# Optimization experiments

Hardware: AMD Instinct MI355X
Metric: run time of the kernel (lower is better)

## Reference

```python
import jax, jax.numpy as jnp
import numpy as np

EPS = 1e-9

def setup_inputs() -> dict:
    key = jax.random.key(0)
    k1, k2, k3, k4 = jax.random.split(key, 4)
    B, D, M, R, C = 1024, 16, 4, 4096, 64
    x = jax.random.normal(k1, (B, D), dtype=jnp.float32)
    centers = jax.random.normal(k2, (D, M), dtype=jnp.float32)
    widths = jnp.ones((D, M), dtype=jnp.float32)
    consequents = jax.random.normal(k3, (R, D + 1, C), dtype=jnp.float32)
    rules = jax.random.randint(k4, (R, D), 0, M)  # rule -> MF index per input dim
    return {"x": x, "centers": centers, "widths": widths,
            "consequents": consequents, "rules": rules}

def reference(x, centers, widths, consequents, rules):
    B, D = x.shape
    # Gaussian membership values: [B, D, M]
    mfs = jnp.exp(-(x[:, :, None] - centers[None]) ** 2 / (2.0 * widths[None] ** 2)) + EPS
    # Gather per-rule MFs: rule_mfs[b, d, r] = mfs[b, d, rules[r, d]] -> [B, D, R]
    rule_mfs = jnp.take_along_axis(mfs, rules.T[None, :, :], axis=2)
    # Product firing strengths and normalization: [B, R]
    fs = jnp.prod(rule_mfs, axis=1)
    nfs = fs / (fs.sum(axis=1, keepdims=True) + EPS)
    # Extended input with bias: [B, D+1]
    x_ext = jnp.concatenate([x, jnp.ones((B, 1), dtype=x.dtype)], axis=1)
    # NOTE: faithful to the original torch code: 'bi,rjc->brc' has no shared
    # contraction index, so it sums x_ext over i and consequents over j.
    rule_out = jnp.einsum('br,brc->bc', nfs,
                          jnp.einsum('bi,rjc->brc', x_ext, consequents))
    return rule_out, nfs, x_ext
```

## Files before the change

### kernel.cpp

```cpp
#include <hip/hip_runtime.h>
#include <hip/hip_bf16.h>

typedef __attribute__((ext_vector_type(8))) short short8;
typedef __attribute__((ext_vector_type(4))) short short4v;
typedef __attribute__((ext_vector_type(4))) float floatx4;
typedef __attribute__((ext_vector_type(4))) unsigned int uintx4;
typedef __attribute__((ext_vector_type(4))) int intx4;
typedef unsigned int u32;
typedef unsigned short u16;

#define NB 1024
#define ND 16
#define NM 4
#define NR 4096
#define NC 64
#define EPSF 1e-9f
#define KSPLIT 32

__device__ inline u16 f2bf(float f) {
    u32 u;
    __builtin_memcpy(&u, &f, 4);
    u32 lsb = (u >> 16) & 1;
    u += 0x7fffu + lsb;
    return (u16)(u >> 16);
}

__global__ __launch_bounds__(256) void k_pack(const int* __restrict__ rules,
                                              u32* __restrict__ packed) {
    int r = blockIdx.x * 256 + threadIdx.x;
    const int* q = rules + (size_t)r * ND;
    u32 pk = 0;
#pragma unroll
    for (int i = 0; i < 4; ++i) {
        intx4 v = *(const intx4*)(q + i * 4);
#pragma unroll
        for (int e = 0; e < 4; ++e) pk |= ((u32)(v[e] & 3)) << (2 * (i * 4 + e));
    }
    packed[r] = pk;
}

__global__ __launch_bounds__(256) void k_mid(const float* __restrict__ cons,
                                             const float* __restrict__ x,
                                             const float* __restrict__ centers,
                                             const float* __restrict__ widths,
                                             const u32* __restrict__ packed,
                                             u16* __restrict__ s_consT,
                                             float* __restrict__ out_nfs,
                                             u16* __restrict__ fs_bf,
                                             float* __restrict__ out_xe,
                                             float* __restrict__ rowscale) {
    __shared__ u16 tile[16][68];
    __shared__ float xv[16];
    __shared__ float mftab[64];
    __shared__ float gtab[1024];
    __shared__ float wred[4];
    __shared__ float s_inv;
    int bid = blockIdx.x;
    int tid = threadIdx.x;
    if (bid < 256) {
        int rbase = bid * 16;
        int c = tid & 63;
        int rr = tid >> 6;
#pragma unroll
        for (int it = 0; it < 4; ++it, rr += 4) {
            const float* p = cons + (size_t)(rbase + rr) * (ND + 1) * NC + c;
            float s = 0.f;
#pragma unroll
            for (int j = 0; j < ND + 1; ++j) s += p[j * NC];
            tile[rr][c] = f2bf(s);
        }
        __syncthreads();
        int cc = tid >> 2;
        int r0 = (tid & 3) * 4;
        short4v v;
#pragma unroll
        for (int e = 0; e < 4; ++e) v[e] = (short)tile[r0 + e][cc];
        *(short4v*)(s_consT + (size_t)cc * NR + rbase + r0) = v;
        return;
    }
    int b = bid - 256;
    uintx4 p[4];
#pragma unroll
    for (int it = 0; it < 4; ++it) p[it] = *(const uintx4*)(packed + it * 1024 + tid * 4);
    if (tid < 16) {
        float raw = x[b * 16 + tid];
        xv[tid] = raw;
        out_xe[b * 17 + tid] = raw;
    }
    if (tid == 16) out_xe[b * 17 + 16] = 1.0f;
    __syncthreads();
    if (tid < 64) {
        float diff = xv[tid >> 2] - centers[tid];
        float w = widths[tid];
        mftab[tid] = __expf(-diff * diff / (2.f * w * w)) + EPSF;
    }
    __syncthreads();
    for (int idx = tid; idx < 1024; idx += 256) {
        int g = idx >> 8, i = idx & 255;
        const float* mf = mftab + g * 16;
        gtab[idx] = mf[0 + (i & 3)] * mf[4 + ((i >> 2) & 3)] *
                    mf[8 + ((i >> 4) & 3)] * mf[12 + ((i >> 6) & 3)];
    }
    __syncthreads();
    floatx4 f[4];
    float lsum = 0.f;
#pragma unroll
    for (int it = 0; it < 4; ++it) {
#pragma unroll
        for (int e = 0; e < 4; ++e) {
            u32 pk = p[it][e];
            f[it][e] = gtab[pk & 255] * gtab[256 + ((pk >> 8) & 255)] *
                       gtab[512 + ((pk >> 16) & 255)] * gtab[768 + (pk >> 24)];
            lsum += f[it][e];
        }
    }
    for (int off = 32; off; off >>= 1) lsum += __shfl_down(lsum, off, 64);
    if ((tid & 63) == 0) wred[tid >> 6] = lsum;
    __syncthreads();
    if (tid == 0) s_inv = 1.f / (wred[0] + wred[1] + wred[2] + wred[3] + EPSF);
    __syncthreads();
    float inv = s_inv;
    if (tid == 0) {
        float s = 1.f;
        for (int i = 0; i < 16; ++i) s += xv[i];
        rowscale[b] = s * inv;
    }
    float* on = out_nfs + (size_t)b * NR;
    u16* ob = fs_bf + (size_t)b * NR;
#pragma unroll
    for (int it = 0; it < 4; ++it) {
        int r = it * 1024 + tid * 4;
        floatx4 v;
        short4v bv;
#pragma unroll
        for (int e = 0; e < 4; ++e) {
            v[e] = f[it][e] * inv;
            bv[e] = (short)f2bf(f[it][e]);
        }
        *(floatx4*)(on + r) = v;
        *(short4v*)(ob + r) = bv;
    }
}

__global__ __launch_bounds__(256) void k_gemm(const u16* __restrict__ fs_bf,
                                              const u16* __restrict__ s_consT,
                                              u16* __restrict__ part) {
    int rt = blockIdx.x;
    int ks = blockIdx.y;
    int tid = threadIdx.x;
    int wid = tid >> 6, lane = tid & 63;
    int arow = rt * 64 + wid * 16 + (lane & 15);
    int kbase = ks * (NR / KSPLIT) + (lane >> 4) * 8;
    const u16* aptr = fs_bf + (size_t)arow * NR + kbase;
    const u16* bptr = s_consT + (size_t)(lane & 15) * NR + kbase;
    short8 A[4], B[4][4];
#pragma unroll
    for (int t = 0; t < 4; ++t) A[t] = *(const short8*)(aptr + t * 32);
#pragma unroll
    for (int cb = 0; cb < 4; ++cb)
#pragma unroll
        for (int t = 0; t < 4; ++t)
            B[cb][t] = *(const short8*)(bptr + (size_t)cb * 16 * NR + t * 32);
    floatx4 acc[4] = {};
#pragma unroll
    for (int t = 0; t < 4; ++t)
#pragma unroll
        for (int cb = 0; cb < 4; ++cb)
            acc[cb] = __builtin_amdgcn_mfma_f32_16x16x32_bf16(A[t], B[cb][t], acc[cb], 0, 0, 0);
    u16* po = part + (size_t)ks * (NB * NC);
    int row0 = rt * 64 + wid * 16 + (lane >> 4) * 4;
#pragma unroll
    for (int cb = 0; cb < 4; ++cb)
#pragma unroll
        for (int reg = 0; reg < 4; ++reg)
            po[(size_t)(row0 + reg) * NC + cb * 16 + (lane & 15)] = f2bf(acc[cb][reg]);
}

__global__ __launch_bounds__(256) void k_out(const u16* __restrict__ part,
                                             const float* __restrict__ rowscale,
                                             float* __restrict__ out0) {
    int t = blockIdx.x * 256 + threadIdx.x;
    float a = 0.f;
#pragma unroll
    for (int ks = 0; ks < KSPLIT; ++ks) {
        u32 u = ((u32)part[(size_t)ks * (NB * NC) + t]) << 16;
        float v;
        __builtin_memcpy(&v, &u, 4);
        a += v;
    }
    out0[t] = a * rowscale[t >> 6];
}

extern "C" void kernel_launch(void* const* d_in, const int* in_sizes, int n_in,
                              void* d_out, int out_size, void* d_ws, size_t ws_size,
                              hipStream_t stream) {
    const float* x = (const float*)d_in[0];
    const float* centers = (const float*)d_in[1];
    const float* widths = (const float*)d_in[2];
    const float* cons = (const float*)d_in[3];
    const int* rules = (const int*)d_in[4];

    float* out = (float*)d_out;
    float* out_rule = out;
    float* out_nfs = out + NB * NC;
    float* out_xe = out + NB * NC + NB * NR;

    char* ws = (char*)d_ws;
    u16* s_consT = (u16*)ws;
    u32* packed = (u32*)(ws + (512 << 10));
    float* rowscale = (float*)(ws + (512 << 10) + (16 << 10));
    u16* fs_bf = (u16*)(ws + (512 << 10) + (24 << 10));
    u16* part = (u16*)(ws + (512 << 10) + (24 << 10) + (size_t)NB * NR * 2);

    k_pack<<<NR / 256, 256, 0, stream>>>(rules, packed);
    k_mid<<<256 + NB, 256, 0, stream>>>(cons, x, centers, widths, packed,
                                        s_consT, out_nfs, fs_bf, out_xe, rowscale);
    k_gemm<<<dim3(16, KSPLIT), 256, 0, stream>>>(fs_bf, s_consT, part);
    k_out<<<(NB * NC) / 256, 256, 0, stream>>>(part, rowscale, out_rule);
}
```

Baseline: 31.71 us.

## Replace split-K partial buffer and reduce kernel with float atomics

The GEMM kernel now scales each split-K partial by the row scale and atomically adds it into the zero-initialised fp32 output, which removes the bf16 partial buffer and the separate reduction kernel. The rule-packing kernel is merged with the consequent-sum kernel, which also zeroes the output, and the firing-strength computation becomes its own kernel. Kernel launches and partial-buffer traffic go down, in exchange for 32-way atomic contention per output element and a nondeterministic summation order. It also gives up the overlap between the consequent reduction and the firing-strength blocks that the old combined kernel had.

```diff
diff --git a/kernel.cpp b/kernel.cpp
--- a/kernel.cpp
+++ b/kernel.cpp
@@ -25,60 +25,64 @@
     return (u16)(u >> 16);
 }
 
-__global__ __launch_bounds__(256) void k_pack(const int* __restrict__ rules,
-                                              u32* __restrict__ packed) {
-    int r = blockIdx.x * 256 + threadIdx.x;
-    const int* q = rules + (size_t)r * ND;
-    u32 pk = 0;
-#pragma unroll
-    for (int i = 0; i < 4; ++i) {
-        intx4 v = *(const intx4*)(q + i * 4);
-#pragma unroll
-        for (int e = 0; e < 4; ++e) pk |= ((u32)(v[e] & 3)) << (2 * (i * 4 + e));
-    }
-    packed[r] = pk;
-}
-
-__global__ __launch_bounds__(256) void k_mid(const float* __restrict__ cons,
-                                             const float* __restrict__ x,
-                                             const float* __restrict__ centers,
-                                             const float* __restrict__ widths,
-                                             const u32* __restrict__ packed,
-                                             u16* __restrict__ s_consT,
-                                             float* __restrict__ out_nfs,
-                                             u16* __restrict__ fs_bf,
-                                             float* __restrict__ out_xe,
-                                             float* __restrict__ rowscale) {
+__global__ __launch_bounds__(256) void k_prep(const float* __restrict__ cons,
+                                              const int* __restrict__ rules,
+                                              u16* __restrict__ s_consT,
+                                              u32* __restrict__ packed,
+                                              float* __restrict__ out_rule) {
     __shared__ u16 tile[16][68];
+    int bid = blockIdx.x;
+    int tid = threadIdx.x;
+    int gt = bid * 256 + tid;
+    if (gt < NB * NC) out_rule[gt] = 0.f;
+    if (bid >= 256) {
+        int r = (bid - 256) * 256 + tid;
+        const int* q = rules + (size_t)r * ND;
+        u32 pk = 0;
+#pragma unroll
+        for (int i = 0; i < 4; ++i) {
+            intx4 v = *(const intx4*)(q + i * 4);
+#pragma unroll
+            for (int e = 0; e < 4; ++e) pk |= ((u32)(v[e] & 3)) << (2 * (i * 4 + e));
+        }
+        packed[r] = pk;
+        return;
+    }
+    int rbase = bid * 16;
+    int c = tid & 63;
+    int rr = tid >> 6;
+#pragma unroll
+    for (int it = 0; it < 4; ++it, rr += 4) {
+        const float* p = cons + (size_t)(rbase + rr) * (ND + 1) * NC + c;
+        float s = 0.f;
+#pragma unroll
+        for (int j = 0; j < ND + 1; ++j) s += p[j * NC];
+        tile[rr][c] = f2bf(s);
+    }
+    __syncthreads();
+    int cc = tid >> 2;
+    int r0 = (tid & 3) * 4;
+    short4v v;
+#pragma unroll
+    for (int e = 0; e < 4; ++e) v[e] = (short)tile[r0 + e][cc];
+    *(short4v*)(s_consT + (size_t)cc * NR + rbase + r0) = v;
+}
+
+__global__ __launch_bounds__(256) void k_fs(const float* __restrict__ x,
+                                            const float* __restrict__ centers,
+                                            const float* __restrict__ widths,
+                                            const u32* __restrict__ packed,
+                                            float* __restrict__ out_nfs,
+                                            u16* __restrict__ fs_bf,
+                                            float* __restrict__ out_xe,
+                                            float* __restrict__ rowscale) {
     __shared__ float xv[16];
     __shared__ float mftab[64];
     __shared__ float gtab[1024];
     __shared__ float wred[4];
     __shared__ float s_inv;
-    int bid = blockIdx.x;
+    int b = blockIdx.x;
     int tid = threadIdx.x;
-    if (bid < 256) {
-        int rbase = bid * 16;
-        int c = tid & 63;
-        int rr = tid >> 6;
-#pragma unroll
-        for (int it = 0; it < 4; ++it, rr += 4) {
-            const float* p = cons + (size_t)(rbase + rr) * (ND + 1) * NC + c;
-            float s = 0.f;
-#pragma unroll
-            for (int j = 0; j < ND + 1; ++j) s += p[j * NC];
-            tile[rr][c] = f2bf(s);
-        }
-        __syncthreads();
-        int cc = tid >> 2;
-        int r0 = (tid & 3) * 4;
-        short4v v;
-#pragma unroll
-        for (int e = 0; e < 4; ++e) v[e] = (short)tile[r0 + e][cc];
-        *(short4v*)(s_consT + (size_t)cc * NR + rbase + r0) = v;
-        return;
-    }
-    int b = bid - 256;
     uintx4 p[4];
 #pragma unroll
     for (int it = 0; it < 4; ++it) p[it] = *(const uintx4*)(packed + it * 1024 + tid * 4);
@@ -144,7 +148,8 @@
 
 __global__ __launch_bounds__(256) void k_gemm(const u16* __restrict__ fs_bf,
                                               const u16* __restrict__ s_consT,
-                                              u16* __restrict__ part) {
+                                              const float* __restrict__ rowscale,
+                                              float* __restrict__ out_rule) {
     int rt = blockIdx.x;
     int ks = blockIdx.y;
     int tid = threadIdx.x;
@@ -167,28 +172,16 @@
 #pragma unroll
         for (int cb = 0; cb < 4; ++cb)
             acc[cb] = __builtin_amdgcn_mfma_f32_16x16x32_bf16(A[t], B[cb][t], acc[cb], 0, 0, 0);
-    u16* po = part + (size_t)ks * (NB * NC);
     int row0 = rt * 64 + wid * 16 + (lane >> 4) * 4;
+    float s4[4];
+#pragma unroll
+    for (int reg = 0; reg < 4; ++reg) s4[reg] = rowscale[row0 + reg];
 #pragma unroll
     for (int cb = 0; cb < 4; ++cb)
 #pragma unroll
         for (int reg = 0; reg < 4; ++reg)
-            po[(size_t)(row0 + reg) * NC + cb * 16 + (lane & 15)] = f2bf(acc[cb][reg]);
-}
-
-__global__ __launch_bounds__(256) void k_out(const u16* __restrict__ part,
-                                             const float* __restrict__ rowscale,
-                                             float* __restrict__ out0) {
-    int t = blockIdx.x * 256 + threadIdx.x;
-    float a = 0.f;
-#pragma unroll
-    for (int ks = 0; ks < KSPLIT; ++ks) {
-        u32 u = ((u32)part[(size_t)ks * (NB * NC) + t]) << 16;
-        float v;
-        __builtin_memcpy(&v, &u, 4);
-        a += v;
-    }
-    out0[t] = a * rowscale[t >> 6];
+            atomicAdd(out_rule + (size_t)(row0 + reg) * NC + cb * 16 + (lane & 15),
+                      acc[cb][reg] * s4[reg]);
 }
 
 extern "C" void kernel_launch(void* const* d_in, const int* in_sizes, int n_in,
@@ -210,11 +203,9 @@
     u32* packed = (u32*)(ws + (512 << 10));
     float* rowscale = (float*)(ws + (512 << 10) + (16 << 10));
     u16* fs_bf = (u16*)(ws + (512 << 10) + (24 << 10));
-    u16* part = (u16*)(ws + (512 << 10) + (24 << 10) + (size_t)NB * NR * 2);
-
-    k_pack<<<NR / 256, 256, 0, stream>>>(rules, packed);
-    k_mid<<<256 + NB, 256, 0, stream>>>(cons, x, centers, widths, packed,
-                                        s_consT, out_nfs, fs_bf, out_xe, rowscale);
-    k_gemm<<<dim3(16, KSPLIT), 256, 0, stream>>>(fs_bf, s_consT, part);
-    k_out<<<(NB * NC) / 256, 256, 0, stream>>>(part, rowscale, out_rule);
-}
+
+    k_prep<<<272, 256, 0, stream>>>(cons, rules, s_consT, packed, out_rule);
+    k_fs<<<NB, 256, 0, stream>>>(x, centers, widths, packed, out_nfs, fs_bf,
+                                 out_xe, rowscale);
+    k_gemm<<<dim3(16, KSPLIT), 256, 0, stream>>>(fs_bf, s_consT, rowscale, out_rule);
+}
```

Result: no change. 31.44 us (median of 2 runs) (-0.9%).
